# Kernel tuning notes

Measured on AMD Instinct MI355X. Metric: run time of the kernel, lower is better.

## Reference

```python
import jax, jax.numpy as jnp
import numpy as np
from jax import lax

B, N, FIN, T = 16, 1024, 32, 24
K, CC, CT = 3, 64, 64   # cheb order, nb_chev_filter, nb_time_filter
EPS = 1e-5


def setup_inputs() -> dict:
    key = jax.random.key(0)
    ks = jax.random.split(key, 16)
    g = lambda i, shape, sc=1.0: jax.random.normal(ks[i], shape, jnp.float32) * sc
    return dict(
        x=g(0, (B, N, FIN, T)),
        # spatial attention params
        W1=g(1, (T,), 0.1), W2=g(2, (FIN, T), 0.1), W3=g(3, (FIN,), 0.1),
        # temporal attention params
        U1=g(4, (N,), 0.03), U2=g(5, (FIN, N), 0.03), U3=g(6, (FIN,), 0.1),
        # Chebyshev polynomials T_k (K,N,N) and Theta (K,F_in,C_chev)
        cheb=g(7, (K, N, N), 1.0 / np.sqrt(N)),
        Theta=g(8, (K, FIN, CC), 1.0 / np.sqrt(FIN)),
        # time conv (1,3) stride (1,1) pad (0,1), residual conv (1,1)
        tc_w=g(9, (CT, CC, 1, 3), 1.0 / np.sqrt(3 * CC)), tc_b=g(10, (CT,), 0.01),
        rc_w=g(11, (CT, FIN, 1, 1), 1.0 / np.sqrt(FIN)), rc_b=g(12, (CT,), 0.01),
        gamma=jnp.ones((CT,), jnp.float32), beta=jnp.zeros((CT,), jnp.float32),
    )


def _layer_norm(z, gamma, beta):
    mu = jnp.mean(z, axis=-1, keepdims=True)
    var = jnp.mean(jnp.square(z - mu), axis=-1, keepdims=True)
    return (z - mu) * lax.rsqrt(var + EPS) * gamma + beta


def reference(x, W1, W2, W3, U1, U2, U3, cheb, Theta, tc_w, tc_b, rc_w, rc_b, gamma, beta):
    # ---- temporal attention: (B,T,T), softmax over axis=1 (as in torch dim=1)
    lhs_t = jnp.einsum('bnft,n->btf', x, U1) @ U2            # (B,T,N)
    rhs_t = jnp.einsum('f,bnft->bnt', U3, x)                 # (B,N,T)
    E = jax.nn.softmax(jnp.einsum('btn,bns->bts', lhs_t, rhs_t), axis=1)  # (B,T,T)

    # x_TAt = reshape(B,N*F,T) @ E, reshaped back
    x_TAt = jnp.einsum('bnft,bts->bnfs', x, E)               # (B,N,F,T)

    # ---- spatial attention on x_TAt: (B,N,N), softmax over axis=1
    lhs_s = jnp.einsum('bnft,t->bnf', x_TAt, W1) @ W2        # (B,N,T)
    rhs_s = jnp.einsum('f,bnft->btn', W3, x_TAt)             # (B,T,N)
    S = jax.nn.softmax(jnp.einsum('bnt,btm->bnm', lhs_s, rhs_s), axis=1)  # (B,N,N)

    # ---- K-order Chebyshev graph conv with spatial attention, fused over T and K
    # rhs[k,b,m,f,t] = sum_n (T_k[n,m]*S[b,n,m]) * x[b,n,f,t]
    Tk_at = cheb[:, None] * S[None]                          # (K,B,N,N)
    rhs = jnp.einsum('kbnm,bnft->kbmft', Tk_at, x)           # (K,B,N,F,T)
    spatial_gcn = jax.nn.relu(jnp.einsum('kbmft,kfo->bmot', rhs, Theta))  # (B,N,CC,T)

    # ---- time conv (1,3) pad (0,1) on (B,CC,N,T)
    dn = ('NCHW', 'OIHW', 'NCHW')
    tco = lax.conv_general_dilated(spatial_gcn.transpose(0, 2, 1, 3), tc_w,
                                   window_strides=(1, 1), padding=[(0, 0), (1, 1)],
                                   dimension_numbers=dn) + tc_b[None, :, None, None]
    # ---- residual 1x1 conv on (B,F,N,T)
    res = lax.conv_general_dilated(x.transpose(0, 2, 1, 3), rc_w,
                                   window_strides=(1, 1), padding=[(0, 0), (0, 0)],
                                   dimension_numbers=dn) + rc_b[None, :, None, None]

    z = jax.nn.relu(res + tco)                               # (B,CT,N,T)
    z = _layer_norm(z.transpose(0, 3, 2, 1), gamma, beta)    # (B,T,N,CT), LN over CT
    return z.transpose(0, 2, 3, 1)                           # (B,N,CT,T)
```

## Files before the change

kernel.cpp:

```cpp
#include <hip/hip_runtime.h>
#include <hip/hip_bf16.h>
#include <math.h>


namespace {

constexpr int B = 16, N = 1024, F = 32, T = 24, CC = 64, CT = 64;
constexpr int FT = F * T;
constexpr int CTT = CT * T;
constexpr int NSEG = 8;

using f32x4  = __attribute__((ext_vector_type(4))) float;
using short8 = __attribute__((ext_vector_type(8))) short;

__device__ __forceinline__ float b2f(__hip_bfloat16 v) { return __bfloat162float(v); }
__device__ __forceinline__ unsigned short f2bu(float x) {
  union { float f; unsigned u; } c; c.f = x;
  unsigned u = c.u;
  return (unsigned short)((u + 0x7FFFu + ((u >> 16) & 1u)) >> 16);
}
__device__ __forceinline__ float us2f(unsigned short u) {
  union { unsigned u; float f; } c; c.u = ((unsigned)u) << 16; return c.f;
}
__device__ __forceinline__ void gload16(const void* g, void* l) {
  __builtin_amdgcn_global_load_lds(
      (const __attribute__((address_space(1))) unsigned int*)g,
      (__attribute__((address_space(3))) unsigned int*)l, 16, 0, 0);
}

__global__ void k_lhs_t(const float* x, const float* U1, float* lhst) {
  int bi = blockIdx.x;
  int f = bi % F; int t = (bi / F) % T; int b = bi / (F * T);
  int tid = threadIdx.x;
  float acc = 0.f;
  for (int n = tid; n < N; n += 64)
    acc += x[(((size_t)b * N + n) * F + f) * T + t] * U1[n];
  #pragma unroll
  for (int off = 32; off > 0; off >>= 1) acc += __shfl_down(acc, off);
  if (tid == 0) lhst[bi] = acc;
}

__global__ void k_lhs2(const float* lhst, const float* U2, float* lhs2) {
  __shared__ float ls[F];
  int tid = threadIdx.x;
  int id = blockIdx.x * 256 + tid;
  int n = id % N; int bt = id / N;
  if (tid < F) ls[tid] = lhst[bt * F + tid];
  __syncthreads();
  float acc = 0.f;
  #pragma unroll
  for (int f = 0; f < F; ++f) acc += ls[f] * U2[f * N + n];
  lhs2[id] = acc;
}

__global__ void k_fx(const float* x, const float* U3, const float* W3,
                     float* rhst, float* w3x) {
  __shared__ float u3s[F], w3s[F];
  int tid = threadIdx.x;
  if (tid < F) { u3s[tid] = U3[tid]; w3s[tid] = W3[tid]; }
  __syncthreads();
  int id = blockIdx.x * 256 + tid;
  int t = id % T; int bn = id / T;
  float au = 0.f, aw = 0.f;
  #pragma unroll
  for (int f = 0; f < F; ++f) {
    float v = x[((size_t)bn * F + f) * T + t];
    au += u3s[f] * v; aw += w3s[f] * v;
  }
  rhst[id] = au; w3x[id] = aw;
}

__global__ void k_Elog(const float* lhs2, const float* rhst, float* Elog) {
  int bi = blockIdx.x;
  int s = bi % T; int t = (bi / T) % T; int b = bi / (T * T);
  int tid = threadIdx.x;
  float acc = 0.f;
  for (int n = tid; n < N; n += 64)
    acc += lhs2[(b * T + t) * N + n] * rhst[(b * N + n) * T + s];
  #pragma unroll
  for (int off = 32; off > 0; off >>= 1) acc += __shfl_down(acc, off);
  if (tid == 0) Elog[bi] = acc;
}

__global__ void k_Esm(const float* Elog, float* E) {
  int b = blockIdx.x; int s = threadIdx.x;
  if (s >= T) return;
  float mx = -1e30f;
  for (int t = 0; t < T; ++t) mx = fmaxf(mx, Elog[(b * T + t) * T + s]);
  float sum = 0.f;
  for (int t = 0; t < T; ++t) sum += expf(Elog[(b * T + t) * T + s] - mx);
  float inv = 1.f / sum;
  for (int t = 0; t < T; ++t)
    E[(b * T + t) * T + s] = expf(Elog[(b * T + t) * T + s] - mx) * inv;
}

__global__ void k_EW1(const float* E, const float* W1, float* EW1) {
  int b = blockIdx.x; int t = threadIdx.x;
  if (t >= T) return;
  float acc = 0.f;
  for (int s = 0; s < T; ++s) acc += E[(b * T + t) * T + s] * W1[s];
  EW1[b * T + t] = acc;
}

__global__ void k_tmp1x(const float* x, const float* EW1, float* tmp1) {
  __shared__ float ew[T];
  int tid = threadIdx.x;
  int id = blockIdx.x * 256 + tid;
  int b = id / (N * F);
  if (tid < T) ew[tid] = EW1[b * T + tid];
  __syncthreads();
  const float* xr = x + (size_t)id * T;
  float acc = 0.f;
  #pragma unroll
  for (int t = 0; t < T; ++t) acc += xr[t] * ew[t];
  tmp1[id] = acc;
}

__global__ void k_lhs_s(const float* tmp1, const float* W2, float* lhss) {
  int id = blockIdx.x * 256 + threadIdx.x;
  int t = id % T; int bn = id / T;
  float acc = 0.f;
  #pragma unroll
  for (int f = 0; f < F; ++f) acc += tmp1[bn * F + f] * W2[f * T + t];
  lhss[id] = acc;
}

__global__ void k_rhss(const float* w3x, const float* E, float* rhss) {
  __shared__ float Ec[T];
  int tid = threadIdx.x;
  int id = blockIdx.x * 256 + tid;
  int m = id % N; int t = (id / N) % T; int b = id / (N * T);
  if (tid < T) Ec[tid] = E[(b * T + tid) * T + t];
  __syncthreads();
  const float* wr = w3x + ((size_t)b * N + m) * T;
  float acc = 0.f;
  #pragma unroll
  for (int tp = 0; tp < T; ++tp) acc += wr[tp] * Ec[tp];
  rhss[id] = acc;
}

__global__ void k_Slog(const float* lhss, const float* rhss, __hip_bfloat16* S) {
  __shared__ float rt[T][256];
  __shared__ float lt[16][T];
  int m0 = blockIdx.x * 256, n0 = blockIdx.y * 16, b = blockIdx.z;
  int tid = threadIdx.x;
  for (int t = 0; t < T; ++t) rt[t][tid] = rhss[((size_t)b * T + t) * N + m0 + tid];
  for (int i = tid; i < 16 * T; i += 256) {
    int n = i / T, t = i % T;
    lt[n][t] = lhss[((size_t)b * N + n0 + n) * T + t];
  }
  __syncthreads();
  #pragma unroll 4
  for (int n = 0; n < 16; ++n) {
    float acc = 0.f;
    #pragma unroll
    for (int t = 0; t < T; ++t) acc += lt[n][t] * rt[t][tid];
    S[((size_t)b * N + n0 + n) * N + m0 + tid] = __float2bfloat16(acc);
  }
}

__global__ __launch_bounds__(256) void k_Ssum(const __hip_bfloat16* S,
                                              float* pmx, float* psm) {
  int m0 = blockIdx.x * 128; int b = blockIdx.y; int z = blockIdx.z;
  int tid = threadIdx.x;
  int lane = tid & 63, nq = tid >> 6;
  int c = m0 + lane * 2;
  float mx0 = -1e30f, sm0 = 0.f, mx1 = -1e30f, sm1 = 0.f;
  #pragma unroll 4
  for (int i = 0; i < 32; ++i) {
    int n = z * 128 + i * 4 + nq;
    unsigned u = *(const unsigned*)&S[((size_t)b * N + n) * N + c];
    float v0 = us2f((unsigned short)(u & 0xffffu));
    float v1 = us2f((unsigned short)(u >> 16));
    float nm0 = fmaxf(mx0, v0);
    sm0 = sm0 * __expf(mx0 - nm0) + __expf(v0 - nm0); mx0 = nm0;
    float nm1 = fmaxf(mx1, v1);
    sm1 = sm1 * __expf(mx1 - nm1) + __expf(v1 - nm1); mx1 = nm1;
  }
  __shared__ float lmx[4][128], lsm[4][128];
  lmx[nq][lane * 2] = mx0; lmx[nq][lane * 2 + 1] = mx1;
  lsm[nq][lane * 2] = sm0; lsm[nq][lane * 2 + 1] = sm1;
  __syncthreads();
  if (nq == 0) {
    #pragma unroll
    for (int cc2 = 0; cc2 < 2; ++cc2) {
      int col = lane * 2 + cc2;
      float M = lmx[0][col], Sg = lsm[0][col];
      #pragma unroll
      for (int s = 1; s < 4; ++s) {
        float m2 = lmx[s][col], s2 = lsm[s][col];
        float nm = fmaxf(M, m2);
        Sg = Sg * __expf(M - nm) + s2 * __expf(m2 - nm);
        M = nm;
      }
      pmx[((size_t)z * B + b) * N + m0 + col] = M;
      psm[((size_t)z * B + b) * N + m0 + col] = Sg;
    }
  }
}

__global__ void k_Scomb(const float* pmx, const float* psm,
                        float* smax, float* sinv) {
  int id = blockIdx.x * 256 + threadIdx.x;
  float M = -1e30f, Sg = 0.f;
  #pragma unroll
  for (int z = 0; z < NSEG; ++z) {
    float m2 = pmx[(size_t)z * B * N + id];
    float s2 = psm[(size_t)z * B * N + id];
    float nm = fmaxf(M, m2);
    Sg = Sg * __expf(M - nm) + s2 * __expf(m2 - nm);
    M = nm;
  }
  smax[id] = M;
  sinv[id] = 1.f / Sg;
}

__global__ __launch_bounds__(256) void k_prepA(const float* cheb,
                                               const __hip_bfloat16* S,
                                               const float* smax,
                                               const float* sinv,
                                               unsigned short* Abf,
                                               int Bc, int b0) {
  __shared__ float Tl[64][65];
  int z = blockIdx.z;
  int k = z / Bc, bl = z % Bc, b = b0 + bl;
  int n0 = blockIdx.x * 64, m0 = blockIdx.y * 64;
  int tid = threadIdx.x;
  int j = tid & 63, i4 = tid >> 6;
  float cm = smax[(size_t)b * N + m0 + j];
  float ci = sinv[(size_t)b * N + m0 + j];
  #pragma unroll
  for (int it = 0; it < 16; ++it) {
    int i = it * 4 + i4;
    Tl[i][j] = cheb[((size_t)k * N + n0 + i) * N + m0 + j] *
               (__expf(b2f(S[((size_t)b * N + n0 + i) * N + m0 + j]) - cm) * ci);
  }
  __syncthreads();
  int i2 = (tid & 31) * 2, j8 = tid >> 5;
  #pragma unroll
  for (int it = 0; it < 8; ++it) {
    int jj = it * 8 + j8;
    unsigned u = (unsigned)f2bu(Tl[i2][jj]) | ((unsigned)f2bu(Tl[i2 + 1][jj]) << 16);
    *(unsigned*)&Abf[((size_t)z * N + m0 + jj) * N + n0 + i2] = u;
  }
}

__global__ __launch_bounds__(256) void k_prepX(const float* x, unsigned short* xT,
                                               int b0) {
  __shared__ float Tl[64][65];
  int bl = blockIdx.z, b = b0 + bl;
  int n0 = blockIdx.x * 64, c0 = blockIdx.y * 64;
  int tid = threadIdx.x;
  int j = tid & 63, i4 = tid >> 6;
  #pragma unroll
  for (int it = 0; it < 16; ++it) {
    int i = it * 4 + i4;
    Tl[i][j] = x[((size_t)b * N + n0 + i) * FT + c0 + j];
  }
  __syncthreads();
  int i2 = (tid & 31) * 2, j8 = tid >> 5;
  #pragma unroll
  for (int it = 0; it < 8; ++it) {
    int jj = it * 8 + j8;
    int c = c0 + jj;
    int row = (c % 24) * 32 + c / 24;
    unsigned u = (unsigned)f2bu(Tl[i2][jj]) | ((unsigned)f2bu(Tl[i2 + 1][jj]) << 16);
    *(unsigned*)&xT[((size_t)bl * FT + row) * N + n0 + i2] = u;
  }
}

__global__ void k_prepW(const float* Theta, const float* tcw, const float* rcw,
                        unsigned short* wbf) {
  int tid = threadIdx.x;
  for (int g = tid; g < 64 * 96; g += 256) {
    int o = g / 96, kk = g % 96;
    wbf[g] = f2bu(Theta[kk * 64 + o]);
  }
  for (int g = tid; g < 64 * 192; g += 256) {
    int o = g / 192, r = g % 192;
    int jj = r / 64, cc = r % 64;
    wbf[6144 + g] = f2bu(tcw[o * 192 + cc * 3 + jj]);
  }
  for (int g = tid; g < 32 * 64; g += 256) {
    int f = g >> 6, o = g & 63;
    wbf[18432 + (f >> 1) * 128 + o * 2 + (f & 1)] = f2bu(rcw[o * 32 + f]);
  }
}

__global__ __launch_bounds__(256) void k_gemm3(const unsigned short* Abf,
                                               const unsigned short* xT,
                                               const unsigned short* wbf,
                                               unsigned short* sg,
                                               int Bc) {
  __shared__ __align__(16) unsigned char smem[53248];
  unsigned short* A_l  = (unsigned short*)smem;
  unsigned short* X_l  = (unsigned short*)(smem + 24576);
  unsigned short* A_th = (unsigned short*)smem;
  int p = blockIdx.x;
  int xcd = p & 7, slot = p >> 3;
  int g = xcd * (2 * Bc) + slot / 6;
  int cx = slot % 6;
  int bl = g >> 4, my = g & 15;
  int m0 = my * 64, c0 = cx * 128;
  int t0 = cx * 4;
  int tid = threadIdx.x;
  int lane = tid & 63, w = tid >> 6;
  int l15 = lane & 15, quad = lane >> 4;
  int wmi = w & 1, wci = w >> 1;
  int nh = lane & 7, ml = lane >> 3;
  int swz = nh ^ ml;

  f32x4 acc[3][2][4];
  #pragma unroll
  for (int k = 0; k < 3; ++k)
    #pragma unroll
    for (int mt = 0; mt < 2; ++mt)
      #pragma unroll
      for (int ct = 0; ct < 4; ++ct) acc[k][mt][ct] = (f32x4){0.f, 0.f, 0.f, 0.f};

  for (int n0 = 0; n0 < N; n0 += 64) {
    #pragma unroll
    for (int it = 0; it < 6; ++it) {
      int k = it >> 1, mh = it & 1;
      int rowb = mh * 32 + w * 8;
      gload16(&Abf[((size_t)(k * Bc + bl) * N + m0 + rowb + ml) * N + n0 + swz * 8],
              &A_l[(k * 64 + rowb) * 64]);
    }
    #pragma unroll
    for (int it = 0; it < 4; ++it) {
      int cb = it * 32 + w * 8;
      gload16(&xT[((size_t)bl * FT + c0 + cb + ml) * N + n0 + swz * 8],
              &X_l[cb * 64]);
    }
    __syncthreads();
    #pragma unroll
    for (int ks = 0; ks < 2; ++ks) {
      short8 bfr[4];
      #pragma unroll
      for (int ct = 0; ct < 4; ++ct) {
        int row = wci * 64 + ct * 16 + l15;
        int pc = (ks * 4 + quad) ^ (row & 7);
        bfr[ct] = *(const short8*)&X_l[row * 64 + pc * 8];
      }
      #pragma unroll
      for (int k = 0; k < 3; ++k)
        #pragma unroll
        for (int mt = 0; mt < 2; ++mt) {
          int row = wmi * 32 + mt * 16 + l15;
          int pc = (ks * 4 + quad) ^ (row & 7);
          short8 af = *(const short8*)&A_l[(k * 64 + row) * 64 + pc * 8];
          #pragma unroll
          for (int ct = 0; ct < 4; ++ct)
            acc[k][mt][ct] = __builtin_amdgcn_mfma_f32_16x16x32_bf16(
                af, bfr[ct], acc[k][mt][ct], 0, 0, 0);
        }
    }
    __syncthreads();
  }

  short8 bth[4][3];
  #pragma unroll
  for (int ot = 0; ot < 4; ++ot)
    #pragma unroll
    for (int ks = 0; ks < 3; ++ks)
      bth[ot][ks] = *(const short8*)&wbf[(ot * 16 + l15) * 96 + ks * 32 + quad * 8];

  #pragma unroll
  for (int k = 0; k < 3; ++k)
    #pragma unroll
    for (int mt = 0; mt < 2; ++mt)
      #pragma unroll
      for (int ct = 0; ct < 4; ++ct) {
        int tl = wci * 2 + (ct >> 1);
        int f  = (ct & 1) * 16 + l15;
        #pragma unroll
        for (int r = 0; r < 4; ++r) {
          int mloc = wmi * 32 + mt * 16 + quad * 4 + r;
          A_th[(mloc * 4 + tl) * 104 + k * 32 + f] = f2bu(acc[k][mt][ct][r]);
        }
      }
  __syncthreads();

  #pragma unroll
  for (int i = 0; i < 4; ++i) {
    short8 af[3];
    #pragma unroll
    for (int ks = 0; ks < 3; ++ks)
      af[ks] = *(const short8*)&A_th[((w * 4 + i) * 16 + l15) * 104 + ks * 32 + quad * 8];
    int mloc = (w * 4 + i) * 4 + quad;
    size_t base = ((size_t)(bl * N + m0 + mloc)) * (T * CC) + (size_t)t0 * CC;
    #pragma unroll
    for (int ot = 0; ot < 4; ++ot) {
      f32x4 th = (f32x4){0.f, 0.f, 0.f, 0.f};
      #pragma unroll
      for (int ks = 0; ks < 3; ++ks)
        th = __builtin_amdgcn_mfma_f32_16x16x32_bf16(af[ks], bth[ot][ks], th, 0, 0, 0);
      #pragma unroll
      for (int rr = 0; rr < 4; ++rr)
        sg[base + (size_t)rr * CC + ot * 16 + l15] = f2bu(fmaxf(th[rr], 0.f));
    }
  }
}

__global__ __launch_bounds__(256) void k_tail(const unsigned short* sg,
                                              const float* x,
                                              const unsigned short* wbf,
                                              const float* tcb, const float* rcb,
                                              const float* gam, const float* bet,
                                              float* out, int b0) {
  __shared__ __align__(16) unsigned char smem[38272];
  float* co_l = (float*)(smem + 13312);
  int tid = threadIdx.x;
  int w = tid >> 6, lane = tid & 63;
  int l15 = lane & 15, quad = lane >> 4;
  int r0l = blockIdx.x * 4;
  int o0 = w * 16;

  short8 btc[6];
  {
    int o = o0 + l15;
    #pragma unroll
    for (int s = 0; s < 6; ++s)
      btc[s] = *(const short8*)&wbf[6144 + o * 192 + s * 32 + quad * 8];
  }

  if (tid < 64) {
    int m = tid >> 4, rr = (tid >> 3) & 1, ck = tid & 7;
    int rp = m * 26 + rr * 25;
    *(uint4*)(smem + rp * 128 + ((ck * 16) ^ ((rp & 7) << 4))) =
        make_uint4(0, 0, 0, 0);
  }
  #pragma unroll
  for (int it = 0; it < 3; ++it) {
    int ch = it * 256 + tid;
    int m = ch / 192, rem = ch % 192;
    int t = rem >> 3, ck = rem & 7;
    uint4 v = *(const uint4*)&sg[((size_t)(r0l + m)) * (T * CC) + t * CC + ck * 8];
    int rp = m * 26 + t + 1;
    *(uint4*)(smem + rp * 128 + ((ck * 16) ^ ((rp & 7) << 4))) = v;
  }
  __syncthreads();

  f32x4 cv[6];
  #pragma unroll
  for (int Mt = 0; Mt < 6; ++Mt) {
    int row = Mt * 16 + l15;
    int m = row / 24, t = row % 24;
    cv[Mt] = (f32x4){0.f, 0.f, 0.f, 0.f};
    #pragma unroll
    for (int s = 0; s < 6; ++s) {
      int rp = m * 26 + t + (s >> 1);
      int cb = (32 * (s & 1) + quad * 8) * 2;
      short8 af = *(const short8*)(smem + rp * 128 + (cb ^ ((rp & 7) << 4)));
      cv[Mt] = __builtin_amdgcn_mfma_f32_16x16x32_bf16(af, btc[s], cv[Mt], 0, 0, 0);
    }
  }
  #pragma unroll
  for (int Mt = 0; Mt < 6; ++Mt)
    #pragma unroll
    for (int r = 0; r < 4; ++r) {
      int row = Mt * 16 + quad * 4 + r;
      co_l[row * 65 + o0 + l15] = cv[Mt][r];
    }
  __syncthreads();

  int o = lane;
  float bias = tcb[o] + rcb[o];
  float acc[T];
  #pragma unroll
  for (int t = 0; t < T; ++t) acc[t] = co_l[(w * 24 + t) * 65 + o] + bias;

  size_t grow = (size_t)b0 * N + r0l + w;
  const float* xrow = x + grow * FT;
  const unsigned* rcp = (const unsigned*)(wbf + 18432);
  #pragma unroll 4
  for (int f2 = 0; f2 < 16; ++f2) {
    unsigned u = rcp[f2 * 64 + o];
    float wf0 = us2f((unsigned short)(u & 0xffffu));
    float wf1 = us2f((unsigned short)(u >> 16));
    const float4* xp0 = (const float4*)&xrow[(f2 * 2) * 24];
    const float4* xp1 = (const float4*)&xrow[(f2 * 2 + 1) * 24];
    #pragma unroll
    for (int q = 0; q < 6; ++q) {
      float4 v0 = xp0[q], v1 = xp1[q];
      acc[q * 4 + 0] += wf0 * v0.x + wf1 * v1.x;
      acc[q * 4 + 1] += wf0 * v0.y + wf1 * v1.y;
      acc[q * 4 + 2] += wf0 * v0.z + wf1 * v1.z;
      acc[q * 4 + 3] += wf0 * v0.w + wf1 * v1.w;
    }
  }
  float g = gam[o], be = bet[o];
  #pragma unroll
  for (int t = 0; t < T; ++t) {
    float z = fmaxf(acc[t], 0.f);
    float s = z, q = z * z;
    #pragma unroll
    for (int off = 1; off < 64; off <<= 1) {
      s += __shfl_xor(s, off);
      q += __shfl_xor(q, off);
    }
    float mu = s * (1.f / 64.f);
    float var = q * (1.f / 64.f) - mu * mu;
    acc[t] = (z - mu) * rsqrtf(var + 1e-5f) * g + be;
  }
  float* orow = out + grow * CTT + o * T;
  #pragma unroll
  for (int q = 0; q < 6; ++q)
    ((float4*)orow)[q] =
        make_float4(acc[q * 4], acc[q * 4 + 1], acc[q * 4 + 2], acc[q * 4 + 3]);
}

}

extern "C" void kernel_launch(void* const* d_in, const int* in_sizes, int n_in,
                              void* d_out, int out_size, void* d_ws, size_t ws_size,
                              hipStream_t stream) {
  (void)in_sizes; (void)n_in; (void)out_size;
  const float* x     = (const float*)d_in[0];
  const float* W1    = (const float*)d_in[1];
  const float* W2    = (const float*)d_in[2];
  const float* W3    = (const float*)d_in[3];
  const float* U1    = (const float*)d_in[4];
  const float* U2    = (const float*)d_in[5];
  const float* U3    = (const float*)d_in[6];
  const float* cheb  = (const float*)d_in[7];
  const float* Theta = (const float*)d_in[8];
  const float* tcw   = (const float*)d_in[9];
  const float* tcb   = (const float*)d_in[10];
  const float* rcw   = (const float*)d_in[11];
  const float* rcb   = (const float*)d_in[12];
  const float* gam   = (const float*)d_in[13];
  const float* bet   = (const float*)d_in[14];
  float* out = (float*)d_out;

  const size_t SB_BYTES = (size_t)B * N * N * 2;
  const size_t WB_BYTES = 65536;
  const size_t AB_PER_B = (size_t)3 * N * N * 2;
  const size_t XT_PER_B = (size_t)FT * N * 2;
  const size_t SG_PER_B = (size_t)N * T * CC * 2;
  const size_t SMALL = 2816384 * 4;
  int Bc = 16;
  while (Bc > 1 && SB_BYTES + WB_BYTES + SMALL +
             (size_t)Bc * (AB_PER_B + XT_PER_B + SG_PER_B) > ws_size)
    Bc >>= 1;

  char* w = (char*)d_ws;
  __hip_bfloat16* Sb = (__hip_bfloat16*)w;
  unsigned short* wbf = (unsigned short*)(w + SB_BYTES);
  unsigned short* Abf = (unsigned short*)(w + SB_BYTES + WB_BYTES);
  unsigned short* xTb = (unsigned short*)(w + SB_BYTES + WB_BYTES +
                                          (size_t)Bc * AB_PER_B);
  unsigned short* sgb = (unsigned short*)(w + SB_BYTES + WB_BYTES +
                                          (size_t)Bc * (AB_PER_B + XT_PER_B));
  float* sm = (float*)(w + SB_BYTES + WB_BYTES +
                       (size_t)Bc * (AB_PER_B + XT_PER_B + SG_PER_B));
  float* lhst = sm;
  float* lhs2 = lhst + B * T * F;
  float* rhst = lhs2 + B * T * N;
  float* w3x  = rhst + B * N * T;
  float* Elog = w3x + B * N * T;
  float* E    = Elog + B * T * T;
  float* EW1  = E + B * T * T;
  float* tmp1 = EW1 + B * T;
  float* lhss = tmp1 + B * N * F;
  float* rhss = lhss + B * N * T;
  float* pmx  = rhss + B * N * T;
  float* psm  = pmx + NSEG * B * N;
  float* smax = psm + NSEG * B * N;
  float* sinv = smax + B * N;

  k_lhs_t<<<B * T * F, 64, 0, stream>>>(x, U1, lhst);
  k_lhs2<<<(B * T * N) / 256, 256, 0, stream>>>(lhst, U2, lhs2);
  k_fx<<<(B * N * T) / 256, 256, 0, stream>>>(x, U3, W3, rhst, w3x);
  k_Elog<<<B * T * T, 64, 0, stream>>>(lhs2, rhst, Elog);
  k_Esm<<<B, 64, 0, stream>>>(Elog, E);
  k_EW1<<<B, 64, 0, stream>>>(E, W1, EW1);

  k_tmp1x<<<(B * N * F) / 256, 256, 0, stream>>>(x, EW1, tmp1);
  k_lhs_s<<<(B * N * T) / 256, 256, 0, stream>>>(tmp1, W2, lhss);
  k_rhss<<<(B * N * T) / 256, 256, 0, stream>>>(w3x, E, rhss);
  k_Slog<<<dim3(N / 256, N / 16, B), 256, 0, stream>>>(lhss, rhss, Sb);
  k_Ssum<<<dim3(N / 128, B, NSEG), 256, 0, stream>>>(Sb, pmx, psm);
  k_Scomb<<<(B * N) / 256, 256, 0, stream>>>(pmx, psm, smax, sinv);

  k_prepW<<<1, 256, 0, stream>>>(Theta, tcw, rcw, wbf);

  for (int b0 = 0; b0 < B; b0 += Bc) {
    k_prepA<<<dim3(N / 64, N / 64, 3 * Bc), 256, 0, stream>>>(cheb, Sb, smax,
                                                              sinv, Abf, Bc, b0);
    k_prepX<<<dim3(N / 64, FT / 64, Bc), 256, 0, stream>>>(x, xTb, b0);
    k_gemm3<<<dim3(96 * Bc), 256, 0, stream>>>(Abf, xTb, wbf, sgb, Bc);
    k_tail<<<Bc * N / 4, 256, 0, stream>>>(sgb, x, wbf, tcb, rcb,
                                           gam, bet, out, b0);
  }
}
```

Measured before the change: 683.3 us.

## Double-buffer the Chebyshev GEMM main loop and fuse E softmax with W1 projection

```diff
diff --git a/kernel.cpp b/kernel.cpp
--- a/kernel.cpp
+++ b/kernel.cpp
@@ -82,24 +82,29 @@
   if (tid == 0) Elog[bi] = acc;
 }
 
-__global__ void k_Esm(const float* Elog, float* E) {
+__global__ void k_EsmW1(const float* Elog, const float* W1,
+                        float* E, float* EW1) {
+  __shared__ float El[T][T + 1];
   int b = blockIdx.x; int s = threadIdx.x;
-  if (s >= T) return;
-  float mx = -1e30f;
-  for (int t = 0; t < T; ++t) mx = fmaxf(mx, Elog[(b * T + t) * T + s]);
-  float sum = 0.f;
-  for (int t = 0; t < T; ++t) sum += expf(Elog[(b * T + t) * T + s] - mx);
-  float inv = 1.f / sum;
-  for (int t = 0; t < T; ++t)
-    E[(b * T + t) * T + s] = expf(Elog[(b * T + t) * T + s] - mx) * inv;
-}
-
-__global__ void k_EW1(const float* E, const float* W1, float* EW1) {
-  int b = blockIdx.x; int t = threadIdx.x;
-  if (t >= T) return;
-  float acc = 0.f;
-  for (int s = 0; s < T; ++s) acc += E[(b * T + t) * T + s] * W1[s];
-  EW1[b * T + t] = acc;
+  if (s < T) {
+    float mx = -1e30f;
+    for (int t = 0; t < T; ++t) mx = fmaxf(mx, Elog[(b * T + t) * T + s]);
+    float sum = 0.f;
+    for (int t = 0; t < T; ++t) sum += expf(Elog[(b * T + t) * T + s] - mx);
+    float inv = 1.f / sum;
+    for (int t = 0; t < T; ++t) {
+      float e = expf(Elog[(b * T + t) * T + s] - mx) * inv;
+      E[(b * T + t) * T + s] = e;
+      El[t][s] = e;
+    }
+  }
+  __syncthreads();
+  int t = threadIdx.x;
+  if (t < T) {
+    float acc = 0.f;
+    for (int s2 = 0; s2 < T; ++s2) acc += El[t][s2] * W1[s2];
+    EW1[b * T + t] = acc;
+  }
 }
 
 __global__ void k_tmp1x(const float* x, const float* EW1, float* tmp1) {
@@ -293,8 +298,10 @@
                                                unsigned short* sg,
                                                int Bc) {
   __shared__ __align__(16) unsigned char smem[53248];
-  unsigned short* A_l  = (unsigned short*)smem;
-  unsigned short* X_l  = (unsigned short*)(smem + 24576);
+  unsigned short* A0 = (unsigned short*)smem;
+  unsigned short* X0 = (unsigned short*)(smem + 12288);
+  unsigned short* A1 = (unsigned short*)(smem + 20480);
+  unsigned short* X1 = (unsigned short*)(smem + 32768);
   unsigned short* A_th = (unsigned short*)smem;
   int p = blockIdx.x;
   int xcd = p & 7, slot = p >> 3;
@@ -307,8 +314,9 @@
   int lane = tid & 63, w = tid >> 6;
   int l15 = lane & 15, quad = lane >> 4;
   int wmi = w & 1, wci = w >> 1;
-  int nh = lane & 7, ml = lane >> 3;
-  int swz = nh ^ ml;
+  int rl = lane >> 2;
+  int ch = (lane & 3) ^ ((rl ^ (rl >> 2)) & 3);
+  int kq = (quad ^ ((l15 ^ (l15 >> 2)) & 3)) * 8;
 
   f32x4 acc[3][2][4];
   #pragma unroll
@@ -318,43 +326,51 @@
       #pragma unroll
       for (int ct = 0; ct < 4; ++ct) acc[k][mt][ct] = (f32x4){0.f, 0.f, 0.f, 0.f};
 
+  auto STAGE = [&](unsigned short* Ab, unsigned short* Xb, int n0s) {
+    #pragma unroll
+    for (int it = 0; it < 3; ++it) {
+      int i = w * 3 + it;
+      int k = i >> 2;
+      int mrow = (i & 3) * 16 + rl;
+      gload16(&Abf[((size_t)(k * Bc + bl) * N + m0 + mrow) * N + n0s + ch * 8],
+              Ab + i * 512);
+    }
+    #pragma unroll
+    for (int it = 0; it < 2; ++it) {
+      int i = w * 2 + it;
+      int crow = i * 16 + rl;
+      gload16(&xT[((size_t)bl * FT + c0 + crow) * N + n0s + ch * 8],
+              Xb + i * 512);
+    }
+  };
+  auto COMPUTE = [&](const unsigned short* Ab, const unsigned short* Xb) {
+    short8 bfr[4];
+    #pragma unroll
+    for (int ct = 0; ct < 4; ++ct) {
+      int row = wci * 64 + ct * 16 + l15;
+      bfr[ct] = *(const short8*)&Xb[row * 32 + kq];
+    }
+    #pragma unroll
+    for (int k = 0; k < 3; ++k)
+      #pragma unroll
+      for (int mt = 0; mt < 2; ++mt) {
+        int row = k * 64 + wmi * 32 + mt * 16 + l15;
+        short8 af = *(const short8*)&Ab[row * 32 + kq];
+        #pragma unroll
+        for (int ct = 0; ct < 4; ++ct)
+          acc[k][mt][ct] = __builtin_amdgcn_mfma_f32_16x16x32_bf16(
+              af, bfr[ct], acc[k][mt][ct], 0, 0, 0);
+      }
+  };
+
+  STAGE(A0, X0, 0);
+  __syncthreads();
   for (int n0 = 0; n0 < N; n0 += 64) {
-    #pragma unroll
-    for (int it = 0; it < 6; ++it) {
-      int k = it >> 1, mh = it & 1;
-      int rowb = mh * 32 + w * 8;
-      gload16(&Abf[((size_t)(k * Bc + bl) * N + m0 + rowb + ml) * N + n0 + swz * 8],
-              &A_l[(k * 64 + rowb) * 64]);
-    }
-    #pragma unroll
-    for (int it = 0; it < 4; ++it) {
-      int cb = it * 32 + w * 8;
-      gload16(&xT[((size_t)bl * FT + c0 + cb + ml) * N + n0 + swz * 8],
-              &X_l[cb * 64]);
-    }
+    STAGE(A1, X1, n0 + 32);
+    COMPUTE(A0, X0);
     __syncthreads();
-    #pragma unroll
-    for (int ks = 0; ks < 2; ++ks) {
-      short8 bfr[4];
-      #pragma unroll
-      for (int ct = 0; ct < 4; ++ct) {
-        int row = wci * 64 + ct * 16 + l15;
-        int pc = (ks * 4 + quad) ^ (row & 7);
-        bfr[ct] = *(const short8*)&X_l[row * 64 + pc * 8];
-      }
-      #pragma unroll
-      for (int k = 0; k < 3; ++k)
-        #pragma unroll
-        for (int mt = 0; mt < 2; ++mt) {
-          int row = wmi * 32 + mt * 16 + l15;
-          int pc = (ks * 4 + quad) ^ (row & 7);
-          short8 af = *(const short8*)&A_l[(k * 64 + row) * 64 + pc * 8];
-          #pragma unroll
-          for (int ct = 0; ct < 4; ++ct)
-            acc[k][mt][ct] = __builtin_amdgcn_mfma_f32_16x16x32_bf16(
-                af, bfr[ct], acc[k][mt][ct], 0, 0, 0);
-        }
-    }
+    if (n0 + 64 < N) STAGE(A0, X0, n0 + 64);
+    COMPUTE(A1, X1);
     __syncthreads();
   }
 
@@ -573,8 +589,7 @@
   k_lhs2<<<(B * T * N) / 256, 256, 0, stream>>>(lhst, U2, lhs2);
   k_fx<<<(B * N * T) / 256, 256, 0, stream>>>(x, U3, W3, rhst, w3x);
   k_Elog<<<B * T * T, 64, 0, stream>>>(lhs2, rhst, Elog);
-  k_Esm<<<B, 64, 0, stream>>>(Elog, E);
-  k_EW1<<<B, 64, 0, stream>>>(E, W1, EW1);
+  k_EsmW1<<<B, 64, 0, stream>>>(Elog, W1, E, EW1);
 
   k_tmp1x<<<(B * N * F) / 256, 256, 0, stream>>>(x, EW1, tmp1);
   k_lhs_s<<<(B * N * T) / 256, 256, 0, stream>>>(tmp1, W2, lhss);
```

After: 667.5 us. 2.3% less time.
